# Kernel optimization log

Measured on AMD Instinct MI355X. Metric: run time of the kernel, lower is better.

Reference implementation:

```python
import jax, jax.numpy as jnp
import numpy as np

NUM_HEADS = 16

def setup_inputs() -> dict:
    key = jax.random.key(0)
    ks = jax.random.split(key, 9)
    E = 1024
    T, B = 2048, 2
    s = E ** -0.5
    return {
        "query": jax.random.normal(ks[0], (T, B, E), dtype=jnp.float32),
        "Wq": jax.random.normal(ks[1], (E, E), dtype=jnp.float32) * s,
        "bq": jax.random.normal(ks[2], (E,), dtype=jnp.float32) * 0.02,
        "Wk": jax.random.normal(ks[3], (E, E), dtype=jnp.float32) * s,
        "bk": jax.random.normal(ks[4], (E,), dtype=jnp.float32) * 0.02,
        "Wv": jax.random.normal(ks[5], (E, E), dtype=jnp.float32) * s,
        "bv": jax.random.normal(ks[6], (E,), dtype=jnp.float32) * 0.02,
        "Wo": jax.random.normal(ks[7], (E, E), dtype=jnp.float32) * s,
        "bo": jax.random.normal(ks[8], (E,), dtype=jnp.float32) * 0.02,
    }

def reference(query, Wq, bq, Wk, bk, Wv, bv, Wo, bo):
    # query: [T, B, E] (seq-first, fairseq/ESM layout)
    T, B, E = query.shape
    H = NUM_HEADS
    D = E // H
    scaling = D ** -0.5
    # projections (eqx Linear: x @ W.T + b); note k/v also come from `query` (self-attention)
    q = (query @ Wq.T + bq) * scaling
    k = query @ Wk.T + bk
    v = query @ Wv.T + bv
    # [T, B, E] -> [B*H, T, D]
    q = q.reshape(T, B * H, D).transpose(1, 0, 2)
    k = k.reshape(T, B * H, D).transpose(1, 0, 2)
    v = v.reshape(T, B * H, D).transpose(1, 0, 2)
    # full score matrix [B*H, T, T], softmax in fp32 (as in original)
    scores = jnp.einsum('ntd,nsd->nts', q, k)
    attn_w = jax.nn.softmax(scores.astype(jnp.float32), axis=-1)
    attn = jnp.einsum('nts,nsd->ntd', attn_w.astype(v.dtype), v)
    # [B*H, T, D] -> [T, B, E]
    attn = attn.transpose(1, 0, 2).reshape(T, B, E)
    return attn @ Wo.T + bo
```

## Files before the change

### kernel.cpp

```cpp
#include <hip/hip_runtime.h>
#include <hip/hip_bf16.h>


typedef __attribute__((ext_vector_type(8))) short short8;
typedef __attribute__((ext_vector_type(4))) float f32x4;
typedef __attribute__((ext_vector_type(16))) float f32x16;
typedef __attribute__((ext_vector_type(4))) unsigned u32x4;

#define T_DIM 2048
#define B_DIM 2
#define E_DIM 1024
#define H_DIM 16
#define D_DIM 64
#define M_ROWS (T_DIM * B_DIM)
#define QKV_N (3 * E_DIM)
#define HEAD_ELEMS (32 * 2048 * 64)
#define LOG2E 1.44269504088896340736f

__device__ __forceinline__ unsigned short f2bf(float f) {
    unsigned u = __builtin_bit_cast(unsigned, f);
    unsigned r = (u + 0x7fffu + ((u >> 16) & 1u)) >> 16;
    return (unsigned short)r;
}

__device__ __forceinline__ unsigned cvt_pk_bf16(float lo, float hi) {
    unsigned d;
    asm("v_cvt_pk_bf16_f32 %0, %1, %2" : "=v"(d) : "v"(lo), "v"(hi));
    return d;
}

__device__ __forceinline__ void gload_lds16(const void* g, void* l) {
    __builtin_amdgcn_global_load_lds(
        (const __attribute__((address_space(1))) void*)g,
        (__attribute__((address_space(3))) void*)l, 16, 0, 0);
}

__device__ __forceinline__ f32x16 mfma32(short8 a, short8 b, f32x16 c) {
    return __builtin_amdgcn_mfma_f32_32x32x16_bf16(a, b, c, 0, 0, 0);
}

__global__ __launch_bounds__(256) void cast_all(
    const float* __restrict__ X,
    const float* __restrict__ Wq, const float* __restrict__ Wk,
    const float* __restrict__ Wv, const float* __restrict__ Wo,
    const float* __restrict__ bq, const float* __restrict__ bk,
    const float* __restrict__ bv,
    unsigned short* __restrict__ Xbf,
    unsigned short* __restrict__ Wcat,
    unsigned short* __restrict__ Wobf,
    float* __restrict__ biasq)
{
    int idx = blockIdx.x * 256 + threadIdx.x;
    if (idx >= (1 << 20)) {
        int i = idx - (1 << 20);
        for (int j = i; j < 3072; j += 256) {
            float v;
            if (j < 1024)       v = 0.125f * LOG2E * bq[j];
            else if (j < 2048)  v = bk[j - 1024];
            else                v = bv[j - 2048];
            biasq[j] = v;
        }
        return;
    }
    size_t base = (size_t)idx * 8;
    int row = (int)(base >> 10);
    int col = (int)(base & 1023);
    const float* src;
    unsigned short* dst;
    float scale = 1.0f;
    if (row < 4096) {
        src = X + base;
        dst = Xbf + base;
    } else if (row < 7168) {
        int wrow = row - 4096;
        if (wrow < 1024)      { src = Wq + ((size_t)wrow << 10) + col; scale = 0.125f * LOG2E; }
        else if (wrow < 2048) { src = Wk + ((size_t)(wrow - 1024) << 10) + col; }
        else                  { src = Wv + ((size_t)(wrow - 2048) << 10) + col; }
        dst = Wcat + ((size_t)wrow << 10) + col;
    } else {
        int wrow = row - 7168;
        src = Wo + ((size_t)wrow << 10) + col;
        dst = Wobf + ((size_t)wrow << 10) + col;
    }
    float4 f0 = *(const float4*)src;
    float4 f1 = *(const float4*)(src + 4);
    short8 r;
    r[0] = (short)f2bf(f0.x * scale);
    r[1] = (short)f2bf(f0.y * scale);
    r[2] = (short)f2bf(f0.z * scale);
    r[3] = (short)f2bf(f0.w * scale);
    r[4] = (short)f2bf(f1.x * scale);
    r[5] = (short)f2bf(f1.y * scale);
    r[6] = (short)f2bf(f1.z * scale);
    r[7] = (short)f2bf(f1.w * scale);
    *(short8*)dst = r;
}

struct GemmCtx {
    const unsigned short* pa0;
    const unsigned short* pa1;
    const unsigned short* pb0;
    const unsigned short* pb1;
    int dofs0, dofs1;
    int wr, wc, lr, lg;
};

__device__ __forceinline__ void gemm_stage(
    GemmCtx& g, unsigned short* Ast, unsigned short* Bst)
{
    gload_lds16(g.pa0, (char*)Ast + g.dofs0);
    gload_lds16(g.pb0, (char*)Bst + g.dofs0);
    gload_lds16(g.pa1, (char*)Ast + g.dofs1);
    gload_lds16(g.pb1, (char*)Bst + g.dofs1);
    g.pa0 += 32; g.pa1 += 32; g.pb0 += 32; g.pb1 += 32;
}

template <bool DO_STAGE, bool LASTWAIT>
__device__ __forceinline__ void gemm_step(
    GemmCtx& g,
    unsigned short* Acs, unsigned short* Bcs,
    unsigned short* Ast, unsigned short* Bst,
    f32x4 (&acc)[4][4])
{
    if constexpr (LASTWAIT) asm volatile("s_waitcnt vmcnt(0)" ::: "memory");
    else                    asm volatile("s_waitcnt vmcnt(4)" ::: "memory");
    __builtin_amdgcn_s_barrier();
    __builtin_amdgcn_sched_barrier(0);
    if constexpr (DO_STAGE) gemm_stage(g, Ast, Bst);

    short8 af[4], bf[4];
#pragma unroll
    for (int m = 0; m < 4; ++m)
        af[m] = *(const short8*)&Acs[(g.wr * 64 + m * 16 + g.lr) * 32 + g.lg * 8];
#pragma unroll
    for (int n = 0; n < 4; ++n)
        bf[n] = *(const short8*)&Bcs[(g.wc * 64 + n * 16 + g.lr) * 32 + g.lg * 8];
    __builtin_amdgcn_s_setprio(1);
#pragma unroll
    for (int m = 0; m < 4; ++m)
#pragma unroll
        for (int n = 0; n < 4; ++n)
            acc[m][n] = __builtin_amdgcn_mfma_f32_16x16x32_bf16(af[m], bf[n], acc[m][n], 0, 0, 0);
    __builtin_amdgcn_s_setprio(0);
}

template <int MODE>
__global__ __launch_bounds__(256) void gemm_bt(
    const unsigned short* __restrict__ A,
    const unsigned short* __restrict__ B,
    const float* __restrict__ bias,
    void* __restrict__ outp,
    int M, int N, int K)
{
    __shared__ alignas(16) unsigned short As[3][128 * 32];
    __shared__ alignas(16) unsigned short Bs[3][128 * 32];
    const int tid = threadIdx.x;
    const int wave = tid >> 6, lane = tid & 63;
    const int lr = lane & 15, lg = lane >> 4;
    const int nbx = N >> 7;
    const int bx = blockIdx.x % nbx, by = blockIdx.x / nbx;
    const int wr = wave >> 1, wc = wave & 1;

    GemmCtx g;
    {
        int c0 = tid, c1 = 256 + tid;
        int r0 = c0 >> 2, k0 = c0 & 3;
        int r1 = c1 >> 2, k1 = c1 & 3;
        g.pa0 = A + (size_t)(by * 128 + r0) * K + k0 * 8;
        g.pb0 = B + (size_t)(bx * 128 + r0) * K + k0 * 8;
        g.pa1 = A + (size_t)(by * 128 + r1) * K + k1 * 8;
        g.pb1 = B + (size_t)(bx * 128 + r1) * K + k1 * 8;
        g.dofs0 = c0 * 16; g.dofs1 = c1 * 16;
        g.wr = wr; g.wc = wc; g.lr = lr; g.lg = lg;
    }
    f32x4 acc[4][4] = {};

    unsigned short *A0 = &As[0][0], *A1 = &As[1][0], *A2 = &As[2][0];
    unsigned short *B0 = &Bs[0][0], *B1 = &Bs[1][0], *B2 = &Bs[2][0];

    gemm_stage(g, A0, B0);
    gemm_stage(g, A1, B1);
#pragma unroll 1
    for (int it = 0; it < 10; ++it) {
        gemm_step<true, false>(g, A0, B0, A2, B2, acc);
        gemm_step<true, false>(g, A1, B1, A0, B0, acc);
        gemm_step<true, false>(g, A2, B2, A1, B1, acc);
    }
    gemm_step<false, false>(g, A0, B0, nullptr, nullptr, acc);
    gemm_step<false, true >(g, A1, B1, nullptr, nullptr, acc);

    const int gcol0 = bx * 128 + wc * 64;
    const int grow0 = by * 128 + wr * 64;
    if (MODE == 0) {
        unsigned short* qb = (unsigned short*)outp;
#pragma unroll
        for (int m = 0; m < 4; ++m) {
#pragma unroll
            for (int n = 0; n < 4; ++n) {
                int col = gcol0 + n * 16 + lr;
                float bsv = bias[col];
                int which = col >> 10;
                int e = col & 1023;
                int h = e >> 6, d = e & 63;
                if (which < 2) {
                    unsigned short* bufb = qb + (size_t)which * HEAD_ELEMS;
#pragma unroll
                    for (int j = 0; j < 4; ++j) {
                        int r = grow0 + m * 16 + lg * 4 + j;
                        int t = r >> 1, b = r & 1;
                        int bh = b * 16 + h;
                        bufb[((size_t)bh * 2048 + t) * 64 + d] = f2bf(acc[m][n][j] + bsv);
                    }
                } else {
                    unsigned* vT32 = (unsigned*)(qb + (size_t)2 * HEAD_ELEMS);
                    int t0 = (grow0 + m * 16 + lg * 4) >> 1;
                    int dwidx = t0 >> 1;
                    int dwp = (dwidx & ~6) | ((dwidx & 2) << 1) | ((dwidx & 4) >> 1);
                    unsigned w0 = (unsigned)f2bf(acc[m][n][0] + bsv) |
                                  ((unsigned)f2bf(acc[m][n][2] + bsv) << 16);
                    unsigned w1 = (unsigned)f2bf(acc[m][n][1] + bsv) |
                                  ((unsigned)f2bf(acc[m][n][3] + bsv) << 16);
                    vT32[(size_t)(h * 64 + d) * 1024 + dwp] = w0;
                    vT32[(size_t)((16 + h) * 64 + d) * 1024 + dwp] = w1;
                }
            }
        }
    } else {
        float* O = (float*)outp;
#pragma unroll
        for (int m = 0; m < 4; ++m) {
#pragma unroll
            for (int n = 0; n < 4; ++n) {
                int col = gcol0 + n * 16 + lr;
                float bsv = bias[col];
#pragma unroll
                for (int j = 0; j < 4; ++j) {
                    int r = grow0 + m * 16 + lg * 4 + j;
                    O[(size_t)r * N + col] = acc[m][n][j] + bsv;
                }
            }
        }
    }
}

struct AttnCtx {
    const unsigned short* pk0;
    const unsigned short* pk1;
    const unsigned short* pv0;
    const unsigned short* pv1;
    int dofs0, dofs1;
    int ql, hi;
};

__device__ __forceinline__ void attn_stage(AttnCtx& cx, char* Kst, char* Vst)
{
    gload_lds16(cx.pk0, Kst + cx.dofs0);
    gload_lds16(cx.pk1, Kst + cx.dofs1);
    gload_lds16(cx.pv0, Vst + cx.dofs0);
    gload_lds16(cx.pv1, Vst + cx.dofs1);
    cx.pk0 += 4096; cx.pk1 += 4096;
    cx.pv0 += 64;   cx.pv1 += 64;
}

template<bool DO_PV, bool DO_STAGE, bool LASTWAIT>
__device__ __forceinline__ void attn_step(
    AttnCtx& cx,
    const char* Kb, const char* Vprv, char* Kst, char* Vst,
    const short8 (&qv)[4],
    const short8 (&paP)[4], short8 (&paC)[4],
    f32x16 (&accO)[2], float& lrun)
{
    const int ql = cx.ql, hi = cx.hi;
    if constexpr (LASTWAIT) asm volatile("s_waitcnt vmcnt(0)" ::: "memory");
    else                    asm volatile("s_waitcnt vmcnt(4)" ::: "memory");
    __builtin_amdgcn_s_barrier();
    __builtin_amdgcn_sched_barrier(0);

    if constexpr (DO_STAGE) attn_stage(cx, Kst, Vst);

    f32x16 st[2] = {};
    __builtin_amdgcn_s_setprio(1);
#pragma unroll
    for (int m = 0; m < 2; ++m) {
        int krow = m * 32 + ql;
#pragma unroll
        for (int c = 0; c < 4; ++c) {
            int bo = (krow * 128 + c * 32 + hi * 16) ^ ((krow & 7) << 4);
            short8 ka = *(const short8*)(Kb + bo);
            st[m] = mfma32(ka, qv[c], st[m]);
        }
    }
    if constexpr (DO_PV) {
#pragma unroll
        for (int n = 0; n < 2; ++n) {
            int d = n * 32 + ql;
#pragma unroll
            for (int kc = 0; kc < 4; ++kc) {
                int bo = (d * 128 + kc * 32 + hi * 16) ^ ((d & 7) << 4);
                short8 va = *(const short8*)(Vprv + bo);
                accO[n] = mfma32(va, paP[kc], accO[n]);
            }
        }
    }
    __builtin_amdgcn_s_setprio(0);
    __builtin_amdgcn_sched_barrier(0);

    float rs0 = 0.f, rs1 = 0.f, rs2 = 0.f, rs3 = 0.f;
#pragma unroll
    for (int m = 0; m < 2; ++m) {
#pragma unroll
        for (int r = 0; r < 16; r += 4) {
            float e0 = __builtin_amdgcn_exp2f(st[m][r + 0]);
            float e1 = __builtin_amdgcn_exp2f(st[m][r + 1]);
            float e2 = __builtin_amdgcn_exp2f(st[m][r + 2]);
            float e3 = __builtin_amdgcn_exp2f(st[m][r + 3]);
            st[m][r + 0] = e0; st[m][r + 1] = e1;
            st[m][r + 2] = e2; st[m][r + 3] = e3;
            rs0 += e0; rs1 += e1; rs2 += e2; rs3 += e3;
        }
    }
    lrun += (rs0 + rs1) + (rs2 + rs3);

#pragma unroll
    for (int kc = 0; kc < 4; ++kc) {
        int m = kc >> 1, b8 = (kc & 1) * 8;
        u32x4 u;
        u[0] = cvt_pk_bf16(st[m][b8 + 0], st[m][b8 + 1]);
        u[1] = cvt_pk_bf16(st[m][b8 + 2], st[m][b8 + 3]);
        u[2] = cvt_pk_bf16(st[m][b8 + 4], st[m][b8 + 5]);
        u[3] = cvt_pk_bf16(st[m][b8 + 6], st[m][b8 + 7]);
        paC[kc] = __builtin_bit_cast(short8, u);
    }
}

__global__ __launch_bounds__(256, 2) void attn_fwd(
    const unsigned short* __restrict__ q,
    const unsigned short* __restrict__ k,
    const unsigned short* __restrict__ vT,
    unsigned short* __restrict__ outb)
{
    __shared__ alignas(16) unsigned short Ks[4][64 * 64];
    __shared__ alignas(16) unsigned short Vs[4][64 * 64];
    const int tid = threadIdx.x, wv = tid >> 6, l = tid & 63;
    const int ql = l & 31, hi = l >> 5;
    const int lid = blockIdx.x;
    const int xcd = lid & 7, slot = lid >> 3;
    const int bh = xcd * 4 + (slot >> 4);
    const int q0 = (slot & 15) * 128;
    const unsigned short* qh = q + (size_t)bh * (2048 * 64);
    const unsigned short* kh = k + (size_t)bh * (2048 * 64);
    const unsigned short* vh = vT + (size_t)bh * (64 * 2048);

    AttnCtx cx;
    {
        int c0 = tid, c1 = 256 + tid;
        int kr0 = c0 >> 3, kr1 = c1 >> 3;
        int ks0 = ((c0 & 7) * 16) ^ ((kr0 & 7) << 4);
        int ks1 = ((c1 & 7) * 16) ^ ((kr1 & 7) << 4);
        cx.pk0 = kh + (size_t)kr0 * 64 + (ks0 >> 1);
        cx.pk1 = kh + (size_t)kr1 * 64 + (ks1 >> 1);
        cx.pv0 = vh + (size_t)kr0 * 2048 + (ks0 >> 1);
        cx.pv1 = vh + (size_t)kr1 * 2048 + (ks1 >> 1);
        cx.dofs0 = c0 * 16; cx.dofs1 = c1 * 16;
        cx.ql = ql; cx.hi = hi;
    }

    char* K0 = (char*)&Ks[0][0]; char* K1 = (char*)&Ks[1][0];
    char* K2 = (char*)&Ks[2][0]; char* K3 = (char*)&Ks[3][0];
    char* V0 = (char*)&Vs[0][0]; char* V1 = (char*)&Vs[1][0];
    char* V2 = (char*)&Vs[2][0]; char* V3 = (char*)&Vs[3][0];

    const int qrow = q0 + wv * 32 + ql;
    short8 qv[4];
#pragma unroll
    for (int c = 0; c < 4; ++c)
        qv[c] = *(const short8*)&qh[(size_t)qrow * 64 + c * 16 + hi * 8];

    f32x16 accO[2] = {};
    float lrun = 0.0f;
    short8 paA[4], paB[4];

    attn_stage(cx, K0, V0);
    attn_stage(cx, K1, V1);

    attn_step<false, true, false>(cx, K0, nullptr, K2, V2,
                                  qv, paB, paA, accO, lrun);
    attn_step<true, true, false>(cx, K1, V0, K3, V3,
                                 qv, paA, paB, accO, lrun);
#pragma unroll 1
    for (int it = 0; it < 7; ++it) {
        attn_step<true, true, false>(cx, K2, V1, K0, V0,
                                     qv, paB, paA, accO, lrun);
        attn_step<true, true, false>(cx, K3, V2, K1, V1,
                                     qv, paA, paB, accO, lrun);
        attn_step<true, true, false>(cx, K0, V3, K2, V2,
                                     qv, paB, paA, accO, lrun);
        attn_step<true, true, false>(cx, K1, V0, K3, V3,
                                     qv, paA, paB, accO, lrun);
    }
    attn_step<true, false, false>(cx, K2, V1, nullptr, nullptr,
                                  qv, paB, paA, accO, lrun);
    attn_step<true, false, true>(cx, K3, V2, nullptr, nullptr,
                                 qv, paA, paB, accO, lrun);
#pragma unroll
    for (int n = 0; n < 2; ++n) {
        int d = n * 32 + ql;
#pragma unroll
        for (int kc = 0; kc < 4; ++kc) {
            int bo = (d * 128 + kc * 32 + hi * 16) ^ ((d & 7) << 4);
            short8 va = *(const short8*)(V3 + bo);
            accO[n] = mfma32(va, paB[kc], accO[n]);
        }
    }

    const float ltot = lrun + __shfl_xor(lrun, 32);
    const float inv = 1.0f / ltot;
    const int b = bh >> 4, h = bh & 15;
    const int orow = qrow * 2 + b;
#pragma unroll
    for (int n = 0; n < 2; ++n)
#pragma unroll
        for (int rq = 0; rq < 4; ++rq) {
            uint2 u;
            u.x = cvt_pk_bf16(accO[n][rq * 4 + 0] * inv, accO[n][rq * 4 + 1] * inv);
            u.y = cvt_pk_bf16(accO[n][rq * 4 + 2] * inv, accO[n][rq * 4 + 3] * inv);
            *(uint2*)&outb[(size_t)orow * 1024 + h * 64 + n * 32 + rq * 8 + hi * 4] = u;
        }
}

extern "C" void kernel_launch(void* const* d_in, const int* in_sizes, int n_in,
                              void* d_out, int out_size, void* d_ws, size_t ws_size,
                              hipStream_t stream) {
    const float* X  = (const float*)d_in[0];
    const float* Wq = (const float*)d_in[1];
    const float* bq = (const float*)d_in[2];
    const float* Wk = (const float*)d_in[3];
    const float* bk = (const float*)d_in[4];
    const float* Wv = (const float*)d_in[5];
    const float* bv = (const float*)d_in[6];
    const float* Wo = (const float*)d_in[7];
    const float* bo = (const float*)d_in[8];
    float* out = (float*)d_out;

    char* ws = (char*)d_ws;
    if (ws_size < ((size_t)49 << 20)) return;
    unsigned short* Xbf   = (unsigned short*)(ws);
    unsigned short* Wcat  = (unsigned short*)(ws + ((size_t)8  << 20));
    unsigned short* Wobf  = (unsigned short*)(ws + ((size_t)14 << 20));
    unsigned short* qb    = (unsigned short*)(ws + ((size_t)16 << 20));
    unsigned short* ab    = (unsigned short*)(ws + ((size_t)40 << 20));
    float*          biasq = (float*)(ws + ((size_t)48 << 20));
    unsigned short* kb  = qb + (size_t)HEAD_ELEMS;
    unsigned short* vTb = qb + (size_t)2 * HEAD_ELEMS;

    cast_all<<<4097, 256, 0, stream>>>(X, Wq, Wk, Wv, Wo, bq, bk, bv,
                                       Xbf, Wcat, Wobf, biasq);
    gemm_bt<0><<<dim3((M_ROWS / 128) * (QKV_N / 128)), 256, 0, stream>>>(
        Xbf, Wcat, biasq, (void*)qb, M_ROWS, QKV_N, E_DIM);
    attn_fwd<<<dim3(32 * 16), 256, 0, stream>>>(qb, kb, vTb, ab);
    gemm_bt<1><<<dim3((M_ROWS / 128) * (E_DIM / 128)), 256, 0, stream>>>(
        ab, Wobf, bo, (void*)out, M_ROWS, E_DIM, E_DIM);
}
```

Measured before the change: 115.7 us.

## Replace QKV projection GEMM with 256x256-tile 8-wave ping-pong kernel

```diff
diff --git a/kernel.cpp b/kernel.cpp
--- a/kernel.cpp
+++ b/kernel.cpp
@@ -96,6 +96,184 @@
     *(short8*)dst = r;
 }
 
+__global__ __launch_bounds__(512, 2) void gemm8p_qkv(
+    const unsigned short* __restrict__ A,
+    const unsigned short* __restrict__ B,
+    const float* __restrict__ bias,
+    unsigned short* __restrict__ qb)
+{
+    __shared__ alignas(16) unsigned short LA[2][2][128 * 64];
+    __shared__ alignas(16) unsigned short LB[2][2][128 * 64];
+    const int tid = threadIdx.x;
+    const int wave = tid >> 6, lane = tid & 63;
+    const int lr = lane & 15, lg = lane >> 4;
+    const int wr = wave >> 2, wc = wave & 3;
+    const int bid = blockIdx.x;
+    const int nb = (bid & 7) * 24 + (bid >> 3);
+    const int bx = nb % 12, by = nb / 12;
+
+    const int lrow = tid >> 3;
+    const int sx = ((tid & 7) * 16) ^ ((lrow & 7) << 4);
+    const unsigned short* pA0 = A + (size_t)(by * 256 + lrow) * 1024 + (sx >> 1);
+    const unsigned short* pB0 = B + (size_t)(bx * 256 + lrow) * 1024 + (sx >> 1);
+    const unsigned short* pA1 = pA0 + (size_t)128 * 1024;
+    const unsigned short* pB1 = pB0 + (size_t)128 * 1024;
+    const int d0 = tid * 16, d1 = (512 + tid) * 16;
+    const size_t ro = (size_t)64 * 1024;
+
+    auto stA0 = [&](int buf) {
+        char* dst = (char*)&LA[buf][0][0];
+        gload_lds16(pA0, dst + d0); gload_lds16(pA0 + ro, dst + d1); pA0 += 64;
+    };
+    auto stA1 = [&](int buf) {
+        char* dst = (char*)&LA[buf][1][0];
+        gload_lds16(pA1, dst + d0); gload_lds16(pA1 + ro, dst + d1); pA1 += 64;
+    };
+    auto stB0 = [&](int buf) {
+        char* dst = (char*)&LB[buf][0][0];
+        gload_lds16(pB0, dst + d0); gload_lds16(pB0 + ro, dst + d1); pB0 += 64;
+    };
+    auto stB1 = [&](int buf) {
+        char* dst = (char*)&LB[buf][1][0];
+        gload_lds16(pB1, dst + d0); gload_lds16(pB1 + ro, dst + d1); pB1 += 64;
+    };
+
+    auto rdA = [&](const unsigned short* base, int m, int kk) -> short8 {
+        int row = m * 16 + lr;
+        int bo = (row * 128 + kk * 64 + lg * 16) ^ ((row & 7) << 4);
+        return *(const short8*)((const char*)base + bo);
+    };
+    auto rdB = [&](const unsigned short* base, int n, int kk) -> short8 {
+        int row = (wc & 1) * 64 + n * 16 + lr;
+        int bo = (row * 128 + kk * 64 + lg * 16) ^ ((row & 7) << 4);
+        return *(const short8*)((const char*)base + bo);
+    };
+
+    f32x4 acc[8][4] = {};
+
+    stA0(0); stA1(0); stB0(0); stB1(0);
+    stA0(1); stA1(1);
+
+#pragma unroll 2
+    for (int kt = 0; kt < 16; ++kt) {
+        const int buf = kt & 1;
+        const unsigned short* Ab = &LA[buf][wr][0];
+        const unsigned short* Bb = &LB[buf][wc >> 1][0];
+        short8 af[8][2], bf[2][2];
+
+        if (kt < 15) stB0(buf ^ 1);
+        if (kt == 0)       asm volatile("s_waitcnt vmcnt(6)" ::: "memory");
+        else if (kt == 15) asm volatile("s_waitcnt vmcnt(0)" ::: "memory");
+        else               asm volatile("s_waitcnt vmcnt(4)" ::: "memory");
+        __builtin_amdgcn_s_barrier();
+        __builtin_amdgcn_sched_barrier(0);
+#pragma unroll
+        for (int m = 0; m < 4; ++m) { af[m][0] = rdA(Ab, m, 0); af[m][1] = rdA(Ab, m, 1); }
+#pragma unroll
+        for (int n = 0; n < 2; ++n) { bf[n][0] = rdB(Bb, n, 0); bf[n][1] = rdB(Bb, n, 1); }
+        asm volatile("s_waitcnt lgkmcnt(0)" ::: "memory");
+        __builtin_amdgcn_sched_barrier(0);
+        __builtin_amdgcn_s_setprio(1);
+#pragma unroll
+        for (int m = 0; m < 4; ++m)
+#pragma unroll
+            for (int n = 0; n < 2; ++n)
+#pragma unroll
+                for (int kk = 0; kk < 2; ++kk)
+                    acc[m][n] = __builtin_amdgcn_mfma_f32_16x16x32_bf16(
+                        af[m][kk], bf[n][kk], acc[m][n], 0, 0, 0);
+        __builtin_amdgcn_s_setprio(0);
+        __builtin_amdgcn_s_barrier();
+
+#pragma unroll
+        for (int m = 4; m < 8; ++m) { af[m][0] = rdA(Ab, m, 0); af[m][1] = rdA(Ab, m, 1); }
+        if (kt < 15) stB1(buf ^ 1);
+        __builtin_amdgcn_s_barrier();
+        asm volatile("s_waitcnt lgkmcnt(0)" ::: "memory");
+        __builtin_amdgcn_sched_barrier(0);
+        __builtin_amdgcn_s_setprio(1);
+#pragma unroll
+        for (int m = 4; m < 8; ++m)
+#pragma unroll
+            for (int n = 0; n < 2; ++n)
+#pragma unroll
+                for (int kk = 0; kk < 2; ++kk)
+                    acc[m][n] = __builtin_amdgcn_mfma_f32_16x16x32_bf16(
+                        af[m][kk], bf[n][kk], acc[m][n], 0, 0, 0);
+        __builtin_amdgcn_s_setprio(0);
+        __builtin_amdgcn_s_barrier();
+
+#pragma unroll
+        for (int n = 0; n < 2; ++n) { bf[n][0] = rdB(Bb, 2 + n, 0); bf[n][1] = rdB(Bb, 2 + n, 1); }
+        if (kt < 14) stA0(buf);
+        __builtin_amdgcn_s_barrier();
+        asm volatile("s_waitcnt lgkmcnt(0)" ::: "memory");
+        __builtin_amdgcn_sched_barrier(0);
+        __builtin_amdgcn_s_setprio(1);
+#pragma unroll
+        for (int m = 4; m < 8; ++m)
+#pragma unroll
+            for (int n = 0; n < 2; ++n)
+#pragma unroll
+                for (int kk = 0; kk < 2; ++kk)
+                    acc[m][2 + n] = __builtin_amdgcn_mfma_f32_16x16x32_bf16(
+                        af[m][kk], bf[n][kk], acc[m][2 + n], 0, 0, 0);
+        __builtin_amdgcn_s_setprio(0);
+        __builtin_amdgcn_s_barrier();
+
+        if (kt < 14) stA1(buf);
+        __builtin_amdgcn_s_barrier();
+        asm volatile("s_waitcnt lgkmcnt(0)" ::: "memory");
+        __builtin_amdgcn_sched_barrier(0);
+        __builtin_amdgcn_s_setprio(1);
+#pragma unroll
+        for (int m = 0; m < 4; ++m)
+#pragma unroll
+            for (int n = 0; n < 2; ++n)
+#pragma unroll
+                for (int kk = 0; kk < 2; ++kk)
+                    acc[m][2 + n] = __builtin_amdgcn_mfma_f32_16x16x32_bf16(
+                        af[m][kk], bf[n][kk], acc[m][2 + n], 0, 0, 0);
+        __builtin_amdgcn_s_setprio(0);
+        __builtin_amdgcn_s_barrier();
+    }
+
+    const int gcol0 = bx * 256 + wc * 64;
+    const int grow0 = by * 256 + wr * 128;
+#pragma unroll
+    for (int m = 0; m < 8; ++m) {
+#pragma unroll
+        for (int n = 0; n < 4; ++n) {
+            int col = gcol0 + n * 16 + lr;
+            float bsv = bias[col];
+            int which = col >> 10;
+            int e = col & 1023;
+            int h = e >> 6, d = e & 63;
+            if (which < 2) {
+                unsigned short* bufb = qb + (size_t)which * HEAD_ELEMS;
+#pragma unroll
+                for (int j = 0; j < 4; ++j) {
+                    int r = grow0 + m * 16 + lg * 4 + j;
+                    int t = r >> 1, b = r & 1;
+                    int bh = b * 16 + h;
+                    bufb[((size_t)bh * 2048 + t) * 64 + d] = f2bf(acc[m][n][j] + bsv);
+                }
+            } else {
+                unsigned* vT32 = (unsigned*)(qb + (size_t)2 * HEAD_ELEMS);
+                int t0 = (grow0 + m * 16 + lg * 4) >> 1;
+                int dwidx = t0 >> 1;
+                int dwp = (dwidx & ~6) | ((dwidx & 2) << 1) | ((dwidx & 4) >> 1);
+                unsigned w0 = (unsigned)f2bf(acc[m][n][0] + bsv) |
+                              ((unsigned)f2bf(acc[m][n][2] + bsv) << 16);
+                unsigned w1 = (unsigned)f2bf(acc[m][n][1] + bsv) |
+                              ((unsigned)f2bf(acc[m][n][3] + bsv) << 16);
+                vT32[(size_t)(h * 64 + d) * 1024 + dwp] = w0;
+                vT32[(size_t)((16 + h) * 64 + d) * 1024 + dwp] = w1;
+            }
+        }
+    }
+}
+
 struct GemmCtx {
     const unsigned short* pa0;
     const unsigned short* pa1;
@@ -144,12 +322,11 @@
     __builtin_amdgcn_s_setprio(0);
 }
 
-template <int MODE>
-__global__ __launch_bounds__(256) void gemm_bt(
+__global__ __launch_bounds__(256) void gemm_out(
     const unsigned short* __restrict__ A,
     const unsigned short* __restrict__ B,
     const float* __restrict__ bias,
-    void* __restrict__ outp,
+    float* __restrict__ O,
     int M, int N, int K)
 {
     __shared__ alignas(16) unsigned short As[3][128 * 32];
@@ -191,53 +368,16 @@
 
     const int gcol0 = bx * 128 + wc * 64;
     const int grow0 = by * 128 + wr * 64;
-    if (MODE == 0) {
-        unsigned short* qb = (unsigned short*)outp;
-#pragma unroll
-        for (int m = 0; m < 4; ++m) {
-#pragma unroll
-            for (int n = 0; n < 4; ++n) {
-                int col = gcol0 + n * 16 + lr;
-                float bsv = bias[col];
-                int which = col >> 10;
-                int e = col & 1023;
-                int h = e >> 6, d = e & 63;
-                if (which < 2) {
-                    unsigned short* bufb = qb + (size_t)which * HEAD_ELEMS;
-#pragma unroll
-                    for (int j = 0; j < 4; ++j) {
-                        int r = grow0 + m * 16 + lg * 4 + j;
-                        int t = r >> 1, b = r & 1;
-                        int bh = b * 16 + h;
-                        bufb[((size_t)bh * 2048 + t) * 64 + d] = f2bf(acc[m][n][j] + bsv);
-                    }
-                } else {
-                    unsigned* vT32 = (unsigned*)(qb + (size_t)2 * HEAD_ELEMS);
-                    int t0 = (grow0 + m * 16 + lg * 4) >> 1;
-                    int dwidx = t0 >> 1;
-                    int dwp = (dwidx & ~6) | ((dwidx & 2) << 1) | ((dwidx & 4) >> 1);
-                    unsigned w0 = (unsigned)f2bf(acc[m][n][0] + bsv) |
-                                  ((unsigned)f2bf(acc[m][n][2] + bsv) << 16);
-                    unsigned w1 = (unsigned)f2bf(acc[m][n][1] + bsv) |
-                                  ((unsigned)f2bf(acc[m][n][3] + bsv) << 16);
-                    vT32[(size_t)(h * 64 + d) * 1024 + dwp] = w0;
-                    vT32[(size_t)((16 + h) * 64 + d) * 1024 + dwp] = w1;
-                }
-            }
-        }
-    } else {
-        float* O = (float*)outp;
-#pragma unroll
-        for (int m = 0; m < 4; ++m) {
-#pragma unroll
-            for (int n = 0; n < 4; ++n) {
-                int col = gcol0 + n * 16 + lr;
-                float bsv = bias[col];
-#pragma unroll
-                for (int j = 0; j < 4; ++j) {
-                    int r = grow0 + m * 16 + lg * 4 + j;
-                    O[(size_t)r * N + col] = acc[m][n][j] + bsv;
-                }
+#pragma unroll
+    for (int m = 0; m < 4; ++m) {
+#pragma unroll
+        for (int n = 0; n < 4; ++n) {
+            int col = gcol0 + n * 16 + lr;
+            float bsv = bias[col];
+#pragma unroll
+            for (int j = 0; j < 4; ++j) {
+                int r = grow0 + m * 16 + lg * 4 + j;
+                O[(size_t)r * N + col] = acc[m][n][j] + bsv;
             }
         }
     }
@@ -455,9 +595,8 @@
 
     cast_all<<<4097, 256, 0, stream>>>(X, Wq, Wk, Wv, Wo, bq, bk, bv,
                                        Xbf, Wcat, Wobf, biasq);
-    gemm_bt<0><<<dim3((M_ROWS / 128) * (QKV_N / 128)), 256, 0, stream>>>(
-        Xbf, Wcat, biasq, (void*)qb, M_ROWS, QKV_N, E_DIM);
+    gemm8p_qkv<<<192, 512, 0, stream>>>(Xbf, Wcat, biasq, qb);
     attn_fwd<<<dim3(32 * 16), 256, 0, stream>>>(qb, kb, vTb, ab);
-    gemm_bt<1><<<dim3((M_ROWS / 128) * (E_DIM / 128)), 256, 0, stream>>>(
-        ab, Wobf, bo, (void*)out, M_ROWS, E_DIM, E_DIM);
-}
+    gemm_out<<<dim3(256), 256, 0, stream>>>(ab, Wobf, bo, out,
+                                            M_ROWS, E_DIM, E_DIM);
+}
```

New measurement: 121.2 us. +4.7%, slower.
